# Optimization experiments

Measured on AMD Instinct MI355X. Metric: run time of the kernel, lower is better.

Reference implementation:

```python
import jax, jax.numpy as jnp
import numpy as np

N_QUBITS = 4
NHEAD = 8


def _normalize_angles(v):
    # per-vector min/max scaling to [0, pi] over last axis (4 elems), as in torch code
    mn = v.min(axis=-1, keepdims=True)
    mx = v.max(axis=-1, keepdims=True)
    return (v - mn) / (mx - mn + 1e-8) * jnp.pi


def _apply_1q(state, U, w):
    # state: [B,H,S,S,2,2,2,2]; apply 2x2 complex gate U on wire w (axis 4+w)
    ax = 4 + w
    s = jnp.moveaxis(state, ax, -1)
    s = s @ U.T  # new[a] = sum_b U[a,b] old[b]
    return jnp.moveaxis(s, -1, ax)


def _apply_cnot(state, c, t):
    ca = 4 + c
    ta = 4 + t - (1 if t > c else 0)  # axis shift after take along ca
    s0 = jnp.take(state, 0, axis=ca)
    s1 = jnp.flip(jnp.take(state, 1, axis=ca), axis=ta)
    return jnp.stack([s0, s1], axis=ca)


def quantum_scores(qa, ka, params):
    # qa, ka: [B,H,S,4] angles in [0,pi]; params: [4]
    # PennyLane: RX(q_w) RZ(k_w) on |0> per wire -> product state, then RX(p_w); CNOT(w, w+1 mod 4); expval Z0
    qh = qa[:, :, :, None, :]  # [B,H,S,1,4] (row index i)
    kh = ka[:, :, None, :, :]  # [B,H,1,S,4] (col index j)
    c = jnp.cos(qh / 2)
    s = jnp.sin(qh / 2)
    amp0 = (c * jnp.exp(-0.5j * kh)).astype(jnp.complex64)   # [B,H,S,S,4]
    amp1 = (-1j * s * jnp.exp(0.5j * kh)).astype(jnp.complex64)
    w = jnp.stack([amp0, amp1], axis=-1)  # [B,H,S,S,4(wire),2(amp)]
    state = jnp.einsum('...a,...b,...c,...d->...abcd',
                       w[..., 0, :], w[..., 1, :], w[..., 2, :], w[..., 3, :])  # [B,H,S,S,2,2,2,2]
    for wq in range(N_QUBITS):
        th = params[wq]
        ct = jnp.cos(th / 2).astype(jnp.complex64)
        st = (-1j * jnp.sin(th / 2)).astype(jnp.complex64)
        U = jnp.stack([jnp.stack([ct, st]), jnp.stack([st, ct])])  # RX(theta)
        state = _apply_1q(state, U, wq)
        state = _apply_cnot(state, wq, (wq + 1) % N_QUBITS)
    probs = state.real ** 2 + state.imag ** 2  # [B,H,S,S,2,2,2,2]
    p = probs.sum(axis=(5, 6, 7))  # marginal over wires 1..3 -> [B,H,S,S,2]
    return p[..., 0] - p[..., 1]   # <Z_0>, [B,H,S,S]


def setup_inputs() -> dict:
    key = jax.random.key(0)
    ks = jax.random.split(key, 10)
    B, S, D = 4, 128, 256
    x = jax.random.normal(ks[0], (B, S, D), dtype=jnp.float32)
    def lin(k):
        kw, kb = jax.random.split(k)
        W = jax.random.normal(kw, (D, D), dtype=jnp.float32) * 0.05
        b = jax.random.normal(kb, (D,), dtype=jnp.float32) * 0.05
        return W, b
    Wq, bq = lin(ks[1]); Wk, bk = lin(ks[2]); Wv, bv = lin(ks[3]); Wo, bo = lin(ks[4])
    attn_params = jax.random.normal(ks[5], (N_QUBITS,), dtype=jnp.float32) * 0.1
    return {"x": x, "Wq": Wq, "bq": bq, "Wk": Wk, "bk": bk,
            "Wv": Wv, "bv": bv, "Wo": Wo, "bo": bo, "attn_params": attn_params}


def reference(x, Wq, bq, Wk, bk, Wv, bv, Wo, bo, attn_params):
    B, S, D = x.shape
    H = NHEAD
    dk = D // H
    Q = (x @ Wq.T + bq).reshape(B, S, H, dk)
    K = (x @ Wk.T + bk).reshape(B, S, H, dk)
    V = (x @ Wv.T + bv).reshape(B, S, H, dk)
    # angles from first n_qubits dims of each head, normalized per (b, i, h)
    qa = jnp.transpose(_normalize_angles(Q[..., :N_QUBITS]), (0, 2, 1, 3))  # [B,H,S,4]
    ka = jnp.transpose(_normalize_angles(K[..., :N_QUBITS]), (0, 2, 1, 3))  # [B,H,S,4]
    scores = quantum_scores(qa, ka, attn_params)  # [B,H,S,S]
    attn = jax.nn.softmax(scores / jnp.sqrt(jnp.float32(dk)), axis=-1)
    Vh = jnp.transpose(V, (0, 2, 1, 3))  # [B,H,S,dk]
    out = jnp.einsum('bhij,bhjd->bhid', attn, Vh)
    out = jnp.transpose(out, (0, 2, 1, 3)).reshape(B, S, D)
    return out @ Wo.T + bo
```

## Files before the change

### kernel.cpp

```cpp
#include <hip/hip_runtime.h>
#include <math.h>

namespace {

constexpr int kB  = 4;
constexpr int kS  = 128;
constexpr int kD  = 256;
constexpr int kH  = 8;
constexpr int kK  = 256;
constexpr float kPi    = 3.14159265358979323846f;
constexpr float kScale = 0.17677669529663687f;

typedef __bf16 bf16x8 __attribute__((ext_vector_type(8)));
typedef float  f32x4  __attribute__((ext_vector_type(4)));

__global__ void convert_xw_kernel(const float* __restrict__ x,
                                  const float* __restrict__ Wq, const float* __restrict__ Wk,
                                  const float* __restrict__ Wv, const float* __restrict__ Wo,
                                  __bf16* __restrict__ xhi, __bf16* __restrict__ xlo,
                                  __bf16* __restrict__ wqkvhi, __bf16* __restrict__ wqkvlo,
                                  __bf16* __restrict__ wohi, __bf16* __restrict__ wolo) {
  const int idx = blockIdx.x * 256 + threadIdx.x;
  float v;
  __bf16 *dh, *dl;
  int o;
  if (idx < 131072) {
    v = x[idx]; dh = xhi; dl = xlo; o = idx;
  } else {
    const int wi = idx - 131072;
    const int m  = wi >> 16;
    const int r  = wi & 65535;
    if (m == 0)      { v = Wq[r]; dh = wqkvhi; dl = wqkvlo; o = wi; }
    else if (m == 1) { v = Wk[r]; dh = wqkvhi; dl = wqkvlo; o = wi; }
    else if (m == 2) { v = Wv[r]; dh = wqkvhi; dl = wqkvlo; o = wi; }
    else             { v = Wo[r]; dh = wohi;   dl = wolo;   o = r;  }
  }
  const __bf16 h = (__bf16)v;
  dh[o] = h;
  dl[o] = (__bf16)(v - (float)h);
}

__global__ void gemm_bf16x3_kernel(const __bf16* __restrict__ ahi, const __bf16* __restrict__ alo,
                                   const __bf16* __restrict__ whi, const __bf16* __restrict__ wlo,
                                   const float* __restrict__ b0, const float* __restrict__ b1,
                                   const float* __restrict__ b2,
                                   float* __restrict__ obase) {
  const int z = blockIdx.z;
  const __bf16* bh = whi + z * 65536;
  const __bf16* bl = wlo + z * 65536;
  const float* bias = (z == 0) ? b0 : (z == 1) ? b1 : b2;
  float* out = obase + z * 131072;

  const int wave = threadIdx.x >> 6;
  const int lane = threadIdx.x & 63;
  const int ln = lane & 15;
  const int qd = lane >> 4;
  const int m0 = blockIdx.x * 16;
  const int n0 = blockIdx.y * 64 + wave * 16;

  const __bf16* ap  = ahi + (m0 + ln) * kK + qd * 8;
  const __bf16* alp = alo + (m0 + ln) * kK + qd * 8;
  const __bf16* bp  = bh  + (n0 + ln) * kK + qd * 8;
  const __bf16* blp = bl  + (n0 + ln) * kK + qd * 8;

  f32x4 acc = {0.f, 0.f, 0.f, 0.f};
#pragma unroll
  for (int kc = 0; kc < kK; kc += 32) {
    const bf16x8 Ah = *(const bf16x8*)(ap  + kc);
    const bf16x8 Al = *(const bf16x8*)(alp + kc);
    const bf16x8 Bh = *(const bf16x8*)(bp  + kc);
    const bf16x8 Bl = *(const bf16x8*)(blp + kc);
    acc = __builtin_amdgcn_mfma_f32_16x16x32_bf16(Ah, Bh, acc, 0, 0, 0);
    acc = __builtin_amdgcn_mfma_f32_16x16x32_bf16(Ah, Bl, acc, 0, 0, 0);
    acc = __builtin_amdgcn_mfma_f32_16x16x32_bf16(Al, Bh, acc, 0, 0, 0);
  }
  const int col  = n0 + ln;
  const float bv = bias[col];
  const int row0 = m0 + qd * 4;
#pragma unroll
  for (int r = 0; r < 4; ++r)
    out[(row0 + r) * kD + col] = acc[r] + bv;
}

__global__ void prep_kernel(const float* __restrict__ Q, const float* __restrict__ K,
                            const float* __restrict__ params,
                            float* __restrict__ qprep,
                            float* __restrict__ kprep) {
  const int idx = blockIdx.x * 256 + threadIdx.x;
  if (idx >= kB * kH * kS) return;
  const int s  = idx & (kS - 1);
  const int bh = idx >> 7;
  const int b  = bh >> 3;
  const int h  = bh & 7;
  const float4 qv = *(const float4*)(Q + (b * kS + s) * kD + h * 32);
  const float4 kv = *(const float4*)(K + (b * kS + s) * kD + h * 32);

  const float qmn = fminf(fminf(qv.x, qv.y), fminf(qv.z, qv.w));
  const float qmx = fmaxf(fmaxf(qv.x, qv.y), fmaxf(qv.z, qv.w));
  const float kmn = fminf(fminf(kv.x, kv.y), fminf(kv.z, kv.w));
  const float kmx = fmaxf(fmaxf(kv.x, kv.y), fmaxf(kv.z, kv.w));
  const float qsc = kPi / (qmx - qmn + 1e-8f);
  const float ksc = kPi / (kmx - kmn + 1e-8f);

  const float qn[3] = {(qv.y - qmn) * qsc, (qv.z - qmn) * qsc, (qv.w - qmn) * qsc};
  const float kn[3] = {(kv.y - kmn) * ksc, (kv.z - kmn) * ksc, (kv.w - kmn) * ksc};

  float* qo = qprep + idx * 8;
  float* ko = kprep + idx * 4;
#pragma unroll
  for (int w = 0; w < 3; ++w) {
    const float th = params[w + 1];
    const float ct = cosf(th), st = sinf(th);
    qo[w]     = ct * cosf(qn[w]);
    qo[w + 3] = st * sinf(qn[w]);
    ko[w]     = cosf(kn[w]);
  }
}

__global__ void fused_attn_kernel(const float* __restrict__ qprep,
                                  const float* __restrict__ kprep,
                                  const float* __restrict__ V,
                                  __bf16* __restrict__ aohi, __bf16* __restrict__ aolo) {
  __shared__ float kC[3][kS];
  __shared__ float Vl[kS][32];
  __shared__ float pl[16][kS + 4];

  const int bh = blockIdx.y;
  const int i0 = blockIdx.x * 16;
  const int b  = bh >> 3;
  const int h  = bh & 7;
  const int tid = threadIdx.x;

  if (tid < kS) {
    const float4 c = *(const float4*)(kprep + (bh * kS + tid) * 4);
    kC[0][tid] = c.x; kC[1][tid] = c.y; kC[2][tid] = c.z;
  }
  {
    const int j0 = tid >> 5, d = tid & 31;
#pragma unroll
    for (int r = 0; r < 16; ++r) {
      const int j = r * 8 + j0;
      Vl[j][d] = V[(b * kS + j) * kD + h * 32 + d];
    }
  }
  __syncthreads();

  const int i_loc = tid >> 4;
  const int jl    = tid & 15;
  const float* qp = qprep + (bh * kS + i0 + i_loc) * 8;
  const float A1 = qp[0], A2 = qp[1], A3 = qp[2];
  const float B1 = qp[3], B2 = qp[4], B3 = qp[5];

  float e[8];
  float mx = -1e30f;
#pragma unroll
  for (int jj = 0; jj < 8; ++jj) {
    const int j = jl + 16 * jj;
    const float v = (A1 - B1 * kC[0][j]) * (A2 - B2 * kC[1][j]) *
                    (A3 - B3 * kC[2][j]) * kScale;
    e[jj] = v;
    mx = fmaxf(mx, v);
  }
#pragma unroll
  for (int m = 1; m < 16; m <<= 1) mx = fmaxf(mx, __shfl_xor(mx, m, 16));
  float sum = 0.f;
#pragma unroll
  for (int jj = 0; jj < 8; ++jj) { e[jj] = expf(e[jj] - mx); sum += e[jj]; }
#pragma unroll
  for (int m = 1; m < 16; m <<= 1) sum += __shfl_xor(sum, m, 16);
  const float inv = 1.f / sum;
#pragma unroll
  for (int jj = 0; jj < 8; ++jj) pl[i_loc][jl + 16 * jj] = e[jj] * inv;
  __syncthreads();

  const int d0 = tid & 15;
  float a0 = 0.f, a1 = 0.f;
#pragma unroll 4
  for (int j = 0; j < kS; ++j) {
    const float p = pl[i_loc][j];
    a0 = fmaf(p, Vl[j][d0], a0);
    a1 = fmaf(p, Vl[j][d0 + 16], a1);
  }
  const int base = (b * kS + i0 + i_loc) * kD + h * 32;
  const __bf16 h0 = (__bf16)a0;
  const __bf16 h1 = (__bf16)a1;
  aohi[base + d0]      = h0;
  aolo[base + d0]      = (__bf16)(a0 - (float)h0);
  aohi[base + d0 + 16] = h1;
  aolo[base + d0 + 16] = (__bf16)(a1 - (float)h1);
}

}

extern "C" void kernel_launch(void* const* d_in, const int* in_sizes, int n_in,
                              void* d_out, int out_size, void* d_ws, size_t ws_size,
                              hipStream_t stream) {
  const float* x  = (const float*)d_in[0];
  const float* Wq = (const float*)d_in[1];
  const float* bq = (const float*)d_in[2];
  const float* Wk = (const float*)d_in[3];
  const float* bk = (const float*)d_in[4];
  const float* Wv = (const float*)d_in[5];
  const float* bv = (const float*)d_in[6];
  const float* Wo = (const float*)d_in[7];
  const float* bo = (const float*)d_in[8];
  const float* pr = (const float*)d_in[9];
  float* out = (float*)d_out;

  float* ws = (float*)d_ws;
  float* Q      = ws;
  float* K      = Q + 131072;
  float* V      = K + 131072;
  float* qprep  = V + 131072;
  float* kprep  = qprep + 32768;
  float* f      = kprep + 16384;
  __bf16* xhi    = (__bf16*)f;
  __bf16* xlo    = xhi + 131072;
  __bf16* wqkvhi = xlo + 131072;
  __bf16* wqkvlo = wqkvhi + 196608;
  __bf16* wohi   = wqkvlo + 196608;
  __bf16* wolo   = wohi + 65536;
  __bf16* aohi   = wolo + 65536;
  __bf16* aolo   = aohi + 131072;

  convert_xw_kernel<<<1536, 256, 0, stream>>>(x, Wq, Wk, Wv, Wo,
                                              xhi, xlo, wqkvhi, wqkvlo, wohi, wolo);
  gemm_bf16x3_kernel<<<dim3(32, 4, 3), 256, 0, stream>>>(xhi, xlo, wqkvhi, wqkvlo,
                                                         bq, bk, bv, Q);
  prep_kernel<<<16, 256, 0, stream>>>(Q, K, pr, qprep, kprep);
  fused_attn_kernel<<<dim3(8, 32), 256, 0, stream>>>(qprep, kprep, V, aohi, aolo);
  gemm_bf16x3_kernel<<<dim3(32, 4, 1), 256, 0, stream>>>(aohi, aolo, wohi, wolo,
                                                         bo, bo, bo, out);
}
```

Baseline: 96.73 us.

## Fuse bf16 split into GEMMs, compute only needed Q/K columns, fold prep into attention

Removes the separate fp32-to-bf16 hi/lo conversion kernel by splitting operands inside the GEMM loops. The QKV projection now computes only the first four columns per head of Q and K, the only ones the scores use, plus the full V. The angle normalisation and trig prep move into the attention kernel's shared-memory setup. This cuts the launch count from five to three and drops most of the Q/K GEMM work, at the cost of redundant per-block splitting and trig.

```diff
diff --git a/kernel.cpp b/kernel.cpp
--- a/kernel.cpp
+++ b/kernel.cpp
@@ -13,117 +13,81 @@
 
 typedef __bf16 bf16x8 __attribute__((ext_vector_type(8)));
 typedef float  f32x4  __attribute__((ext_vector_type(4)));
-
-__global__ void convert_xw_kernel(const float* __restrict__ x,
-                                  const float* __restrict__ Wq, const float* __restrict__ Wk,
-                                  const float* __restrict__ Wv, const float* __restrict__ Wo,
-                                  __bf16* __restrict__ xhi, __bf16* __restrict__ xlo,
-                                  __bf16* __restrict__ wqkvhi, __bf16* __restrict__ wqkvlo,
-                                  __bf16* __restrict__ wohi, __bf16* __restrict__ wolo) {
-  const int idx = blockIdx.x * 256 + threadIdx.x;
-  float v;
-  __bf16 *dh, *dl;
-  int o;
-  if (idx < 131072) {
-    v = x[idx]; dh = xhi; dl = xlo; o = idx;
-  } else {
-    const int wi = idx - 131072;
-    const int m  = wi >> 16;
-    const int r  = wi & 65535;
-    if (m == 0)      { v = Wq[r]; dh = wqkvhi; dl = wqkvlo; o = wi; }
-    else if (m == 1) { v = Wk[r]; dh = wqkvhi; dl = wqkvlo; o = wi; }
-    else if (m == 2) { v = Wv[r]; dh = wqkvhi; dl = wqkvlo; o = wi; }
-    else             { v = Wo[r]; dh = wohi;   dl = wolo;   o = r;  }
-  }
-  const __bf16 h = (__bf16)v;
-  dh[o] = h;
-  dl[o] = (__bf16)(v - (float)h);
-}
-
-__global__ void gemm_bf16x3_kernel(const __bf16* __restrict__ ahi, const __bf16* __restrict__ alo,
-                                   const __bf16* __restrict__ whi, const __bf16* __restrict__ wlo,
-                                   const float* __restrict__ b0, const float* __restrict__ b1,
-                                   const float* __restrict__ b2,
-                                   float* __restrict__ obase) {
-  const int z = blockIdx.z;
-  const __bf16* bh = whi + z * 65536;
-  const __bf16* bl = wlo + z * 65536;
-  const float* bias = (z == 0) ? b0 : (z == 1) ? b1 : b2;
-  float* out = obase + z * 131072;
-
+typedef float  f32x8  __attribute__((ext_vector_type(8)));
+
+__device__ inline void split8(const float* __restrict__ p, bf16x8& hi, bf16x8& lo) {
+  const f32x8 v = *(const f32x8*)p;
+#pragma unroll
+  for (int e = 0; e < 8; ++e) {
+    const __bf16 h = (__bf16)v[e];
+    hi[e] = h;
+    lo[e] = (__bf16)(v[e] - (float)h);
+  }
+}
+
+__global__ void qkv_kernel(const float* __restrict__ x,
+                           const float* __restrict__ Wq, const float* __restrict__ bq,
+                           const float* __restrict__ Wk, const float* __restrict__ bk,
+                           const float* __restrict__ Wv, const float* __restrict__ bv,
+                           float* __restrict__ V, float* __restrict__ Qs,
+                           float* __restrict__ Ks) {
   const int wave = threadIdx.x >> 6;
   const int lane = threadIdx.x & 63;
   const int ln = lane & 15;
   const int qd = lane >> 4;
   const int m0 = blockIdx.x * 16;
-  const int n0 = blockIdx.y * 64 + wave * 16;
-
-  const __bf16* ap  = ahi + (m0 + ln) * kK + qd * 8;
-  const __bf16* alp = alo + (m0 + ln) * kK + qd * 8;
-  const __bf16* bp  = bh  + (n0 + ln) * kK + qd * 8;
-  const __bf16* blp = bl  + (n0 + ln) * kK + qd * 8;
+  const int ny = blockIdx.y;
+
+  const float* W;
+  const float* bias;
+  int wrow;
+  if (ny < 4) {
+    W = Wv; bias = bv;
+    wrow = ny * 64 + wave * 16 + ln;
+  } else {
+    const int c = (wave & 1) * 16 + ln;
+    wrow = (c >> 2) * 32 + (c & 3);
+    if (wave < 2) { W = Wq; bias = bq; } else { W = Wk; bias = bk; }
+  }
+
+  const float* ap = x + (m0 + ln) * kK + qd * 8;
+  const float* bp = W + wrow * kK + qd * 8;
 
   f32x4 acc = {0.f, 0.f, 0.f, 0.f};
 #pragma unroll
   for (int kc = 0; kc < kK; kc += 32) {
-    const bf16x8 Ah = *(const bf16x8*)(ap  + kc);
-    const bf16x8 Al = *(const bf16x8*)(alp + kc);
-    const bf16x8 Bh = *(const bf16x8*)(bp  + kc);
-    const bf16x8 Bl = *(const bf16x8*)(blp + kc);
+    bf16x8 Ah, Al, Bh, Bl;
+    split8(ap + kc, Ah, Al);
+    split8(bp + kc, Bh, Bl);
     acc = __builtin_amdgcn_mfma_f32_16x16x32_bf16(Ah, Bh, acc, 0, 0, 0);
     acc = __builtin_amdgcn_mfma_f32_16x16x32_bf16(Ah, Bl, acc, 0, 0, 0);
     acc = __builtin_amdgcn_mfma_f32_16x16x32_bf16(Al, Bh, acc, 0, 0, 0);
   }
-  const int col  = n0 + ln;
-  const float bv = bias[col];
+  const float bvv = bias[wrow];
   const int row0 = m0 + qd * 4;
-#pragma unroll
-  for (int r = 0; r < 4; ++r)
-    out[(row0 + r) * kD + col] = acc[r] + bv;
-}
-
-__global__ void prep_kernel(const float* __restrict__ Q, const float* __restrict__ K,
-                            const float* __restrict__ params,
-                            float* __restrict__ qprep,
-                            float* __restrict__ kprep) {
-  const int idx = blockIdx.x * 256 + threadIdx.x;
-  if (idx >= kB * kH * kS) return;
-  const int s  = idx & (kS - 1);
-  const int bh = idx >> 7;
-  const int b  = bh >> 3;
-  const int h  = bh & 7;
-  const float4 qv = *(const float4*)(Q + (b * kS + s) * kD + h * 32);
-  const float4 kv = *(const float4*)(K + (b * kS + s) * kD + h * 32);
-
-  const float qmn = fminf(fminf(qv.x, qv.y), fminf(qv.z, qv.w));
-  const float qmx = fmaxf(fmaxf(qv.x, qv.y), fmaxf(qv.z, qv.w));
-  const float kmn = fminf(fminf(kv.x, kv.y), fminf(kv.z, kv.w));
-  const float kmx = fmaxf(fmaxf(kv.x, kv.y), fmaxf(kv.z, kv.w));
-  const float qsc = kPi / (qmx - qmn + 1e-8f);
-  const float ksc = kPi / (kmx - kmn + 1e-8f);
-
-  const float qn[3] = {(qv.y - qmn) * qsc, (qv.z - qmn) * qsc, (qv.w - qmn) * qsc};
-  const float kn[3] = {(kv.y - kmn) * ksc, (kv.z - kmn) * ksc, (kv.w - kmn) * ksc};
-
-  float* qo = qprep + idx * 8;
-  float* ko = kprep + idx * 4;
-#pragma unroll
-  for (int w = 0; w < 3; ++w) {
-    const float th = params[w + 1];
-    const float ct = cosf(th), st = sinf(th);
-    qo[w]     = ct * cosf(qn[w]);
-    qo[w + 3] = st * sinf(qn[w]);
-    ko[w]     = cosf(kn[w]);
-  }
-}
-
-__global__ void fused_attn_kernel(const float* __restrict__ qprep,
-                                  const float* __restrict__ kprep,
+  if (ny < 4) {
+    const int col = ny * 64 + wave * 16 + ln;
+#pragma unroll
+    for (int r = 0; r < 4; ++r)
+      V[(row0 + r) * kD + col] = acc[r] + bvv;
+  } else {
+    const int c = (wave & 1) * 16 + ln;
+    float* o = (wave < 2) ? Qs : Ks;
+#pragma unroll
+    for (int r = 0; r < 4; ++r)
+      o[(row0 + r) * 32 + c] = acc[r] + bvv;
+  }
+}
+
+__global__ void fused_attn_kernel(const float* __restrict__ Qs,
+                                  const float* __restrict__ Ks,
                                   const float* __restrict__ V,
+                                  const float* __restrict__ params,
                                   __bf16* __restrict__ aohi, __bf16* __restrict__ aolo) {
   __shared__ float kC[3][kS];
   __shared__ float Vl[kS][32];
   __shared__ float pl[16][kS + 4];
+  __shared__ float qA[16][3], qB[16][3];
 
   const int bh = blockIdx.y;
   const int i0 = blockIdx.x * 16;
@@ -132,8 +96,26 @@
   const int tid = threadIdx.x;
 
   if (tid < kS) {
-    const float4 c = *(const float4*)(kprep + (bh * kS + tid) * 4);
-    kC[0][tid] = c.x; kC[1][tid] = c.y; kC[2][tid] = c.z;
+    const float4 kv = *(const float4*)(Ks + (b * kS + tid) * 32 + h * 4);
+    const float kmn = fminf(fminf(kv.x, kv.y), fminf(kv.z, kv.w));
+    const float kmx = fmaxf(fmaxf(kv.x, kv.y), fmaxf(kv.z, kv.w));
+    const float ksc = kPi / (kmx - kmn + 1e-8f);
+    kC[0][tid] = cosf((kv.y - kmn) * ksc);
+    kC[1][tid] = cosf((kv.z - kmn) * ksc);
+    kC[2][tid] = cosf((kv.w - kmn) * ksc);
+  } else if (tid < kS + 16) {
+    const int il = tid - kS;
+    const float4 qv = *(const float4*)(Qs + (b * kS + i0 + il) * 32 + h * 4);
+    const float qmn = fminf(fminf(qv.x, qv.y), fminf(qv.z, qv.w));
+    const float qmx = fmaxf(fmaxf(qv.x, qv.y), fmaxf(qv.z, qv.w));
+    const float qsc = kPi / (qmx - qmn + 1e-8f);
+    const float qn[3] = {(qv.y - qmn) * qsc, (qv.z - qmn) * qsc, (qv.w - qmn) * qsc};
+#pragma unroll
+    for (int w = 0; w < 3; ++w) {
+      const float th = params[w + 1];
+      qA[il][w] = cosf(th) * cosf(qn[w]);
+      qB[il][w] = sinf(th) * sinf(qn[w]);
+    }
   }
   {
     const int j0 = tid >> 5, d = tid & 31;
@@ -147,9 +129,8 @@
 
   const int i_loc = tid >> 4;
   const int jl    = tid & 15;
-  const float* qp = qprep + (bh * kS + i0 + i_loc) * 8;
-  const float A1 = qp[0], A2 = qp[1], A3 = qp[2];
-  const float B1 = qp[3], B2 = qp[4], B3 = qp[5];
+  const float A1 = qA[i_loc][0], A2 = qA[i_loc][1], A3 = qA[i_loc][2];
+  const float B1 = qB[i_loc][0], B2 = qB[i_loc][1], B3 = qB[i_loc][2];
 
   float e[8];
   float mx = -1e30f;
@@ -188,6 +169,41 @@
   aolo[base + d0]      = (__bf16)(a0 - (float)h0);
   aohi[base + d0 + 16] = h1;
   aolo[base + d0 + 16] = (__bf16)(a1 - (float)h1);
+}
+
+__global__ void out_gemm_kernel(const __bf16* __restrict__ aohi,
+                                const __bf16* __restrict__ aolo,
+                                const float* __restrict__ Wo,
+                                const float* __restrict__ bo,
+                                float* __restrict__ out) {
+  const int wave = threadIdx.x >> 6;
+  const int lane = threadIdx.x & 63;
+  const int ln = lane & 15;
+  const int qd = lane >> 4;
+  const int m0 = blockIdx.x * 16;
+  const int n0 = blockIdx.y * 64 + wave * 16;
+
+  const __bf16* ap  = aohi + (m0 + ln) * kK + qd * 8;
+  const __bf16* alp = aolo + (m0 + ln) * kK + qd * 8;
+  const float*  bp  = Wo + (n0 + ln) * kK + qd * 8;
+
+  f32x4 acc = {0.f, 0.f, 0.f, 0.f};
+#pragma unroll
+  for (int kc = 0; kc < kK; kc += 32) {
+    const bf16x8 Ah = *(const bf16x8*)(ap  + kc);
+    const bf16x8 Al = *(const bf16x8*)(alp + kc);
+    bf16x8 Bh, Bl;
+    split8(bp + kc, Bh, Bl);
+    acc = __builtin_amdgcn_mfma_f32_16x16x32_bf16(Ah, Bh, acc, 0, 0, 0);
+    acc = __builtin_amdgcn_mfma_f32_16x16x32_bf16(Ah, Bl, acc, 0, 0, 0);
+    acc = __builtin_amdgcn_mfma_f32_16x16x32_bf16(Al, Bh, acc, 0, 0, 0);
+  }
+  const int col  = n0 + ln;
+  const float bv = bo[col];
+  const int row0 = m0 + qd * 4;
+#pragma unroll
+  for (int r = 0; r < 4; ++r)
+    out[(row0 + r) * kD + col] = acc[r] + bv;
 }
 
 }
@@ -208,27 +224,13 @@
   float* out = (float*)d_out;
 
   float* ws = (float*)d_ws;
-  float* Q      = ws;
-  float* K      = Q + 131072;
-  float* V      = K + 131072;
-  float* qprep  = V + 131072;
-  float* kprep  = qprep + 32768;
-  float* f      = kprep + 16384;
-  __bf16* xhi    = (__bf16*)f;
-  __bf16* xlo    = xhi + 131072;
-  __bf16* wqkvhi = xlo + 131072;
-  __bf16* wqkvlo = wqkvhi + 196608;
-  __bf16* wohi   = wqkvlo + 196608;
-  __bf16* wolo   = wohi + 65536;
-  __bf16* aohi   = wolo + 65536;
-  __bf16* aolo   = aohi + 131072;
-
-  convert_xw_kernel<<<1536, 256, 0, stream>>>(x, Wq, Wk, Wv, Wo,
-                                              xhi, xlo, wqkvhi, wqkvlo, wohi, wolo);
-  gemm_bf16x3_kernel<<<dim3(32, 4, 3), 256, 0, stream>>>(xhi, xlo, wqkvhi, wqkvlo,
-                                                         bq, bk, bv, Q);
-  prep_kernel<<<16, 256, 0, stream>>>(Q, K, pr, qprep, kprep);
-  fused_attn_kernel<<<dim3(8, 32), 256, 0, stream>>>(qprep, kprep, V, aohi, aolo);
-  gemm_bf16x3_kernel<<<dim3(32, 4, 1), 256, 0, stream>>>(aohi, aolo, wohi, wolo,
-                                                         bo, bo, bo, out);
-}
+  float* V   = ws;
+  float* Qs  = V + 131072;
+  float* Ks  = Qs + 16384;
+  __bf16* aohi = (__bf16*)(Ks + 16384);
+  __bf16* aolo = aohi + 131072;
+
+  qkv_kernel<<<dim3(32, 5), 256, 0, stream>>>(x, Wq, bq, Wk, bk, Wv, bv, V, Qs, Ks);
+  fused_attn_kernel<<<dim3(8, 32), 256, 0, stream>>>(Qs, Ks, V, pr, aohi, aolo);
+  out_gemm_kernel<<<dim3(32, 4), 256, 0, stream>>>(aohi, aolo, Wo, bo, out);
+}
```

After: 88.09 us. -8.9%, faster.
